# Performance work log

Measured on AMD Instinct MI355X. Metric: run time of the kernel, lower is better.

The kernel has to match this reference:

```python
import jax, jax.numpy as jnp
import numpy as np
import math

IN_CH, KEY_SIZE, VALUE_SIZE = 512, 64, 64
N, T = 4, 4096

def setup_inputs() -> dict:
    key = jax.random.key(0)
    ks = jax.random.split(key, 7)
    s_in = 1.0 / math.sqrt(IN_CH)
    return {
        "x": jax.random.normal(ks[0], (N, T, IN_CH), dtype=jnp.float32),
        "Wq": jax.random.uniform(ks[1], (IN_CH, KEY_SIZE), jnp.float32, -s_in, s_in),
        "bq": jax.random.uniform(ks[2], (KEY_SIZE,), jnp.float32, -s_in, s_in),
        "Wk": jax.random.uniform(ks[3], (IN_CH, KEY_SIZE), jnp.float32, -s_in, s_in),
        "bk": jax.random.uniform(ks[4], (KEY_SIZE,), jnp.float32, -s_in, s_in),
        "Wv": jax.random.uniform(ks[5], (IN_CH, VALUE_SIZE), jnp.float32, -s_in, s_in),
        "bv": jax.random.uniform(ks[6], (VALUE_SIZE,), jnp.float32, -s_in, s_in),
    }

def reference(x, Wq, bq, Wk, bk, Wv, bv):
    # x: [N, T, C]
    Tlen = x.shape[1]
    q = x @ Wq + bq              # [N, T, K]
    k = x @ Wk + bk              # [N, T, K]
    v = x @ Wv + bv              # [N, T, V]
    logits = jnp.einsum('ntk,nsk->nts', q, k)  # [N, T, T]
    # causal mask: strict upper triangle -> -inf (applied BEFORE scaling, as in the original)
    causal = jnp.tril(jnp.ones((Tlen, Tlen), dtype=bool))
    logits = jnp.where(causal, logits, -jnp.inf)
    scale = 1.0 / math.sqrt(Wq.shape[1])
    attn = jax.nn.softmax(logits * scale, axis=-1)
    read = jnp.einsum('nts,nsv->ntv', attn, v)  # [N, T, V]
    return jnp.concatenate((x, read), axis=2)   # [N, T, C+V]
```

## Files before the change

kernel.cpp:

```cpp
#include <hip/hip_runtime.h>
#include <stdint.h>

typedef __attribute__((ext_vector_type(8))) short bf16x8;
typedef __attribute__((ext_vector_type(4))) float f32x4;
typedef __attribute__((ext_vector_type(4))) unsigned short u16x4;
typedef unsigned short u16;

#define NBATCH 4
#define SEQ    4096
#define CIN    512
#define HD     64
#define OC     576
#define NROW   (NBATCH * SEQ)
#define KVB    262144

__device__ __forceinline__ float b2f(u16 u) {
    union { uint32_t i; float f; } w; w.i = ((uint32_t)u) << 16; return w.f;
}
__device__ __forceinline__ u16 f2b(float f) {
    union { float f; uint32_t i; } w; w.f = f;
    uint32_t r = w.i + 0x7fffu + ((w.i >> 16) & 1u);
    return (u16)(r >> 16);
}
__device__ __forceinline__ uint32_t cvtpk_bf16(float a, float b) {
    uint32_t r;
    asm("v_cvt_pk_bf16_f32 %0, %1, %2" : "=v"(r) : "v"(a), "v"(b));
    return r;
}

__global__ void prep_wt(const float* __restrict__ Wq, const float* __restrict__ Wk,
                        const float* __restrict__ Wv, u16* __restrict__ wt) {
    int row = blockIdx.x;
    int g = row >> 6, j = row & 63;
    const float* W = (g == 0) ? Wq : (g == 1) ? Wk : Wv;
    for (int k = threadIdx.x; k < CIN; k += blockDim.x)
        wt[row * CIN + k] = f2b(W[k * HD + j]);
}

__global__ __launch_bounds__(256) void proj(
    const float* __restrict__ x, const u16* __restrict__ wt,
    const float* __restrict__ bq, const float* __restrict__ bk, const float* __restrict__ bv,
    u16* __restrict__ qb, u16* __restrict__ kbuf, u16* __restrict__ vtb,
    float* __restrict__ out)
{
    __shared__ __align__(16) float xs[16 * 512];

    int tid = threadIdx.x;
    int lane = tid & 63, w = tid >> 6;
    int m = lane & 15, quad = lane >> 4;
    int r0 = blockIdx.x * 16;

    {
        int rw = w >> 1;
        int pp = (w & 1) * 64 + lane;
#pragma unroll
        for (int k = 0; k < 8; k++) {
            int r = k * 2 + rw;
            int g = pp ^ (r & 15);
            const float* src = x + (size_t)(r0 + r) * CIN + g * 4;
            float* dst = xs + (size_t)(k * 256 + w * 64 + lane) * 4;
            __builtin_amdgcn_global_load_lds(
                (const __attribute__((address_space(1))) void*)src,
                (__attribute__((address_space(3))) void*)dst, 16, 0, 0);
        }
    }
    __syncthreads();

    int ntb = w * 3;

    f32x4 acc[3];
#pragma unroll
    for (int i = 0; i < 3; i++) acc[i] = (f32x4){0.f, 0.f, 0.f, 0.f};

    const float* xrow = xs + (size_t)m * 512;

#pragma unroll
    for (int c = 0; c < 16; c++) {
        int L0 = c * 8 + quad * 2;
        f32x4 va = *(const f32x4*)(xrow + (size_t)((L0 ^ m) * 4));
        f32x4 vb = *(const f32x4*)(xrow + (size_t)(((L0 + 1) ^ m) * 4));
        bf16x8 a;
#pragma unroll
        for (int j = 0; j < 4; j++) { a[j] = (short)f2b(va[j]); a[4 + j] = (short)f2b(vb[j]); }
#pragma unroll
        for (int t = 0; t < 3; t++) {
            int nt = ntb + t;
            bf16x8 b = *(const bf16x8*)(wt + (size_t)(nt * 16 + m) * CIN + c * 32 + quad * 8);
            acc[t] = __builtin_amdgcn_mfma_f32_16x16x32_bf16(a, b, acc[t], 0, 0, 0);
        }
    }

#pragma unroll
    for (int k = 0; k < 8; k++) {
        int G = k * 256 + tid;
        int r = G >> 7, p = G & 127;
        f32x4 v = *(const f32x4*)(xs + (size_t)G * 4);
        int col = (p ^ (r & 15)) * 4;
        *(f32x4*)(out + (size_t)(r0 + r) * OC + col) = v;
    }

    int n  = r0 >> 12;
    int tl = r0 & (SEQ - 1);

    const float SCQ = 0.125f * 1.44269504088896f;

#pragma unroll
    for (int t = 0; t < 3; t++) {
        int nt = ntb + t;
        int bi = (nt & 3) * 16 + m;
        if (nt < 4) {
            float biasq = bq[bi];
#pragma unroll
            for (int reg = 0; reg < 4; reg++) {
                size_t r = (size_t)(r0 + quad * 4 + reg);
                qb[r * HD + bi] = f2b((acc[t][reg] + biasq) * SCQ);
            }
        } else if (nt < 8) {
            float biask = bk[bi];
            u16* kbase = kbuf + (size_t)n * KVB
                       + (((size_t)(tl >> 4) * 8 + (bi >> 3)) * 16) * 8 + (bi & 7);
#pragma unroll
            for (int reg = 0; reg < 4; reg++) {
                int mkey = quad * 4 + reg;
                kbase[(size_t)mkey * 8] = f2b(acc[t][reg] + biask);
            }
        } else {
            float biasv = bv[bi];
            u16x4 pk;
#pragma unroll
            for (int reg = 0; reg < 4; reg++) pk[reg] = f2b(acc[t][reg] + biasv);
            int key0 = tl + quad * 4;
            size_t off = ((((size_t)(bi >> 4) * 128 + (key0 >> 5)) * 4
                           + ((key0 >> 3) & 3)) * 16 + (bi & 15)) * 8 + (key0 & 7);
            *(u16x4*)(vtb + (size_t)n * KVB + off) = pk;
        }
    }
}

__global__ __launch_bounds__(512, 2) void attn(
    const u16* __restrict__ qb, const u16* __restrict__ kbuf,
    const u16* __restrict__ vtb, float* __restrict__ out)
{
    __shared__ __align__(16) union {
        short p[8][16 * 72];
        float o[8][16][68];
    } lu;
    __shared__ float ldsm[8][16];
    __shared__ float ldsl[8][16];

    int tid = threadIdx.x;
    int lane = tid & 63, w = tid >> 6;
    int m = lane & 15, quad = lane >> 4;

    int idx = blockIdx.x;
    int xcd = idx & 7;
    int batch = xcd >> 1;
    int sub = (idx >> 3) * 2 + (xcd & 1);
    int jj = 127 - sub;
    int t0 = jj * 32;
    int nkb = (jj >> 1) + 1;
    int lastkb = nkb - 1;

    const u16* kpb = kbuf + (size_t)batch * KVB;
    const u16* vpb = vtb + (size_t)batch * KVB;

    bf16x8 ones;
#pragma unroll
    for (int i = 0; i < 8; i++) ones[i] = (short)0x3F80;

    const u16* qpb = qb + (size_t)(batch * SEQ + t0 + m) * HD + quad * 8;
    bf16x8 q0[2], q1[2];
#pragma unroll
    for (int q = 0; q < 2; q++) {
        q0[q] = *(const bf16x8*)(qpb + (size_t)(q * 16) * HD);
        q1[q] = *(const bf16x8*)(qpb + (size_t)(q * 16) * HD + 32);
    }

    float mst[2];
    f32x4 o[2][4], ol[2];
#pragma unroll
    for (int q = 0; q < 2; q++) {
        mst[q] = -1e30f;
        ol[q] = (f32x4){0.f, 0.f, 0.f, 0.f};
#pragma unroll
        for (int nt = 0; nt < 4; nt++) o[q][nt] = (f32x4){0.f, 0.f, 0.f, 0.f};
    }

    int cnt = (nkb > w) ? ((nkb - w + 7) >> 3) : 0;
    int kb = w;
    short* pw = &lu.p[w][0];

    bf16x8 k0[4], k1[4];
#pragma unroll
    for (int st = 0; st < 4; st++) {
        k0[st] = *(const bf16x8*)(kpb + (size_t)((kb * 4 + st) * 8 + quad) * 128 + m * 8);
        k1[st] = *(const bf16x8*)(kpb + (size_t)((kb * 4 + st) * 8 + quad + 4) * 128 + m * 8);
    }

    for (int it = 0; it < cnt; it++, kb += 8) {
        int s0 = kb * 64;
        bool diag = (kb == lastkb);

        bf16x8 vf0[4], vf1[4];
#pragma unroll
        for (int nt = 0; nt < 4; nt++) {
            vf0[nt] = *(const bf16x8*)(vpb + (size_t)((nt * 128 + (s0 >> 5)) * 4 + quad) * 128 + m * 8);
            vf1[nt] = *(const bf16x8*)(vpb + (size_t)((nt * 128 + (s0 >> 5) + 1) * 4 + quad) * 128 + m * 8);
        }

        f32x4 s[2][4];
#pragma unroll
        for (int q = 0; q < 2; q++)
#pragma unroll
            for (int st = 0; st < 4; st++) {
                f32x4 a = (f32x4){0.f, 0.f, 0.f, 0.f};
                a = __builtin_amdgcn_mfma_f32_16x16x32_bf16(k0[st], q0[q], a, 0, 0, 0);
                a = __builtin_amdgcn_mfma_f32_16x16x32_bf16(k1[st], q1[q], a, 0, 0, 0);
                s[q][st] = a;
            }

        if (it + 1 < cnt) {
            int kn = kb + 8;
#pragma unroll
            for (int st = 0; st < 4; st++) {
                k0[st] = *(const bf16x8*)(kpb + (size_t)((kn * 4 + st) * 8 + quad) * 128 + m * 8);
                k1[st] = *(const bf16x8*)(kpb + (size_t)((kn * 4 + st) * 8 + quad + 4) * 128 + m * 8);
            }
        }

        if (diag) {
#pragma unroll
            for (int q = 0; q < 2; q++)
#pragma unroll
                for (int st = 0; st < 4; st++)
#pragma unroll
                    for (int r = 0; r < 4; r++) {
                        int key = s0 + st * 16 + quad * 4 + r;
                        if (key > t0 + q * 16 + m) s[q][st][r] = -1e30f;
                    }
        }

        bf16x8 pf0[2], pf1[2];
#pragma unroll
        for (int q = 0; q < 2; q++) {
            float mx = -1e30f;
#pragma unroll
            for (int st = 0; st < 4; st++) {
                float a01 = fmaxf(s[q][st][0], s[q][st][1]);
                float a23 = fmaxf(s[q][st][2], s[q][st][3]);
                mx = fmaxf(mx, fmaxf(a01, a23));
            }
            mx = fmaxf(mx, __shfl_xor(mx, 16, 64));
            mx = fmaxf(mx, __shfl_xor(mx, 32, 64));

            if (__any(mx > mst[q] + 8.0f)) {
                float mn = fmaxf(mst[q], mx);
                float al = exp2f(mst[q] - mn);
#pragma unroll
                for (int nt = 0; nt < 4; nt++)
#pragma unroll
                    for (int r = 0; r < 4; r++) o[q][nt][r] *= al;
                ol[q][0] *= al;
                mst[q] = mn;
            }

#pragma unroll
            for (int st = 0; st < 4; st++) {
                float e0 = exp2f(s[q][st][0] - mst[q]);
                float e1 = exp2f(s[q][st][1] - mst[q]);
                float e2 = exp2f(s[q][st][2] - mst[q]);
                float e3 = exp2f(s[q][st][3] - mst[q]);
                uint2 pk2;
                pk2.x = cvtpk_bf16(e0, e1);
                pk2.y = cvtpk_bf16(e2, e3);
                *(uint2*)(pw + m * 72 + st * 16 + quad * 4) = pk2;
            }
            __asm__ volatile("" ::: "memory");
            pf0[q] = *(const bf16x8*)(pw + m * 72 + quad * 8);
            pf1[q] = *(const bf16x8*)(pw + m * 72 + 32 + quad * 8);
            __asm__ volatile("" ::: "memory");
        }

#pragma unroll
        for (int q = 0; q < 2; q++) {
#pragma unroll
            for (int nt = 0; nt < 4; nt++) {
                o[q][nt] = __builtin_amdgcn_mfma_f32_16x16x32_bf16(vf0[nt], pf0[q], o[q][nt], 0, 0, 0);
                o[q][nt] = __builtin_amdgcn_mfma_f32_16x16x32_bf16(vf1[nt], pf1[q], o[q][nt], 0, 0, 0);
            }
            ol[q] = __builtin_amdgcn_mfma_f32_16x16x32_bf16(ones, pf0[q], ol[q], 0, 0, 0);
            ol[q] = __builtin_amdgcn_mfma_f32_16x16x32_bf16(ones, pf1[q], ol[q], 0, 0, 0);
        }
    }

    __syncthreads();

#pragma unroll
    for (int q = 0; q < 2; q++) {
        if (quad == 0) { ldsm[w][m] = mst[q]; ldsl[w][m] = ol[q][0]; }
#pragma unroll
        for (int nt = 0; nt < 4; nt++)
            *(f32x4*)&lu.o[w][m][nt * 16 + quad * 4] = o[q][nt];
        __syncthreads();

        if (tid < 256) {
            int t = tid >> 4, vg = tid & 15;
            float mmax = -1e30f;
#pragma unroll
            for (int u = 0; u < 8; u++) mmax = fmaxf(mmax, ldsm[u][t]);
            float L = 0.f;
            f32x4 acc = (f32x4){0.f, 0.f, 0.f, 0.f};
#pragma unroll
            for (int u = 0; u < 8; u++) {
                float c = exp2f(ldsm[u][t] - mmax);
                L += ldsl[u][t] * c;
                f32x4 ov = *(const f32x4*)&lu.o[u][t][vg * 4];
#pragma unroll
                for (int i2 = 0; i2 < 4; i2++) acc[i2] += ov[i2] * c;
            }
            float inv = 1.0f / L;
            f32x4 res;
#pragma unroll
            for (int i2 = 0; i2 < 4; i2++) res[i2] = acc[i2] * inv;
            *(f32x4*)(out + (size_t)(batch * SEQ + t0 + q * 16 + t) * OC + CIN + vg * 4) = res;
        }
        __syncthreads();
    }
}

extern "C" void kernel_launch(void* const* d_in, const int* in_sizes, int n_in,
                              void* d_out, int out_size, void* d_ws, size_t ws_size,
                              hipStream_t stream) {
    const float* x  = (const float*)d_in[0];
    const float* Wq = (const float*)d_in[1];
    const float* bq = (const float*)d_in[2];
    const float* Wk = (const float*)d_in[3];
    const float* bk = (const float*)d_in[4];
    const float* Wv = (const float*)d_in[5];
    const float* bv = (const float*)d_in[6];
    float* out = (float*)d_out;

    u16* ws  = (u16*)d_ws;
    u16* wt  = ws;
    u16* qb  = ws + 131072;
    u16* kb  = qb + 16384 * 64;
    u16* vtb = kb + 16384 * 64;

    prep_wt<<<dim3(192), dim3(256), 0, stream>>>(Wq, Wk, Wv, wt);
    proj<<<dim3(1024), dim3(256), 0, stream>>>(x, wt, bq, bk, bv, qb, kb, vtb, out);
    attn<<<dim3(512), dim3(512), 0, stream>>>(qb, kb, vtb, out);
}
```

Baseline: 140.6 us.

## Process 32 rows per projection block and retile weights for coalesced MFMA loads

The projection kernel now handles 32 rows per block instead of 16, so each loaded weight fragment feeds two MFMAs and weight traffic is halved. The bf16 weight matrix is rearranged in prep_wt so each MFMA B-operand load is contiguous across lanes. The fp32-to-bf16 conversion uses packed v_cvt_pk_bf16_f32 instructions. In exchange, LDS use doubles to 64KB per block and the grid halves, which lowers occupancy and parallelism.

New measurement: 129.1 us. 8.2% less time.

```diff
diff --git a/kernel.cpp b/kernel.cpp
--- a/kernel.cpp
+++ b/kernel.cpp
@@ -33,8 +33,12 @@
     int row = blockIdx.x;
     int g = row >> 6, j = row & 63;
     const float* W = (g == 0) ? Wq : (g == 1) ? Wk : Wv;
-    for (int k = threadIdx.x; k < CIN; k += blockDim.x)
-        wt[row * CIN + k] = f2b(W[k * HD + j]);
+    int nt = row >> 4, m = row & 15;
+    for (int k = threadIdx.x; k < CIN; k += blockDim.x) {
+        int c = k >> 5, qd = (k >> 3) & 3, jj = k & 7;
+        size_t off = ((size_t)(nt * 16 + c) * 64 + qd * 16 + m) * 8 + jj;
+        wt[off] = f2b(W[k * HD + j]);
+    }
 }
 
 __global__ __launch_bounds__(256) void proj(
@@ -43,21 +47,21 @@
     u16* __restrict__ qb, u16* __restrict__ kbuf, u16* __restrict__ vtb,
     float* __restrict__ out)
 {
-    __shared__ __align__(16) float xs[16 * 512];
+    __shared__ __align__(16) float xs[32 * 512];
 
     int tid = threadIdx.x;
     int lane = tid & 63, w = tid >> 6;
     int m = lane & 15, quad = lane >> 4;
-    int r0 = blockIdx.x * 16;
+    int r0b = blockIdx.x * 32;
 
     {
         int rw = w >> 1;
         int pp = (w & 1) * 64 + lane;
 #pragma unroll
-        for (int k = 0; k < 8; k++) {
+        for (int k = 0; k < 16; k++) {
             int r = k * 2 + rw;
             int g = pp ^ (r & 15);
-            const float* src = x + (size_t)(r0 + r) * CIN + g * 4;
+            const float* src = x + (size_t)(r0b + r) * CIN + g * 4;
             float* dst = xs + (size_t)(k * 256 + w * 64 + lane) * 4;
             __builtin_amdgcn_global_load_lds(
                 (const __attribute__((address_space(1))) void*)src,
@@ -68,71 +72,92 @@
 
     int ntb = w * 3;
 
-    f32x4 acc[3];
-#pragma unroll
-    for (int i = 0; i < 3; i++) acc[i] = (f32x4){0.f, 0.f, 0.f, 0.f};
-
-    const float* xrow = xs + (size_t)m * 512;
+    f32x4 acc0[3], acc1[3];
+#pragma unroll
+    for (int i = 0; i < 3; i++) {
+        acc0[i] = (f32x4){0.f, 0.f, 0.f, 0.f};
+        acc1[i] = (f32x4){0.f, 0.f, 0.f, 0.f};
+    }
+
+    const float* xrow0 = xs + (size_t)m * 512;
+    const float* xrow1 = xs + (size_t)(16 + m) * 512;
 
 #pragma unroll
     for (int c = 0; c < 16; c++) {
         int L0 = c * 8 + quad * 2;
-        f32x4 va = *(const f32x4*)(xrow + (size_t)((L0 ^ m) * 4));
-        f32x4 vb = *(const f32x4*)(xrow + (size_t)(((L0 + 1) ^ m) * 4));
-        bf16x8 a;
-#pragma unroll
-        for (int j = 0; j < 4; j++) { a[j] = (short)f2b(va[j]); a[4 + j] = (short)f2b(vb[j]); }
+        f32x4 va0 = *(const f32x4*)(xrow0 + (size_t)((L0 ^ m) * 4));
+        f32x4 vb0 = *(const f32x4*)(xrow0 + (size_t)(((L0 + 1) ^ m) * 4));
+        f32x4 va1 = *(const f32x4*)(xrow1 + (size_t)((L0 ^ m) * 4));
+        f32x4 vb1 = *(const f32x4*)(xrow1 + (size_t)(((L0 + 1) ^ m) * 4));
+        bf16x8 a0, a1;
+        {
+            uint32_t* p0 = (uint32_t*)&a0;
+            p0[0] = cvtpk_bf16(va0[0], va0[1]);
+            p0[1] = cvtpk_bf16(va0[2], va0[3]);
+            p0[2] = cvtpk_bf16(vb0[0], vb0[1]);
+            p0[3] = cvtpk_bf16(vb0[2], vb0[3]);
+            uint32_t* p1 = (uint32_t*)&a1;
+            p1[0] = cvtpk_bf16(va1[0], va1[1]);
+            p1[1] = cvtpk_bf16(va1[2], va1[3]);
+            p1[2] = cvtpk_bf16(vb1[0], vb1[1]);
+            p1[3] = cvtpk_bf16(vb1[2], vb1[3]);
+        }
 #pragma unroll
         for (int t = 0; t < 3; t++) {
             int nt = ntb + t;
-            bf16x8 b = *(const bf16x8*)(wt + (size_t)(nt * 16 + m) * CIN + c * 32 + quad * 8);
-            acc[t] = __builtin_amdgcn_mfma_f32_16x16x32_bf16(a, b, acc[t], 0, 0, 0);
-        }
-    }
-
-#pragma unroll
-    for (int k = 0; k < 8; k++) {
+            bf16x8 b = *(const bf16x8*)(wt + ((size_t)(nt * 16 + c) * 64 + quad * 16 + m) * 8);
+            acc0[t] = __builtin_amdgcn_mfma_f32_16x16x32_bf16(a0, b, acc0[t], 0, 0, 0);
+            acc1[t] = __builtin_amdgcn_mfma_f32_16x16x32_bf16(a1, b, acc1[t], 0, 0, 0);
+        }
+    }
+
+#pragma unroll
+    for (int k = 0; k < 16; k++) {
         int G = k * 256 + tid;
         int r = G >> 7, p = G & 127;
         f32x4 v = *(const f32x4*)(xs + (size_t)G * 4);
         int col = (p ^ (r & 15)) * 4;
-        *(f32x4*)(out + (size_t)(r0 + r) * OC + col) = v;
-    }
-
-    int n  = r0 >> 12;
-    int tl = r0 & (SEQ - 1);
+        *(f32x4*)(out + (size_t)(r0b + r) * OC + col) = v;
+    }
 
     const float SCQ = 0.125f * 1.44269504088896f;
 
 #pragma unroll
-    for (int t = 0; t < 3; t++) {
-        int nt = ntb + t;
-        int bi = (nt & 3) * 16 + m;
-        if (nt < 4) {
-            float biasq = bq[bi];
-#pragma unroll
-            for (int reg = 0; reg < 4; reg++) {
-                size_t r = (size_t)(r0 + quad * 4 + reg);
-                qb[r * HD + bi] = f2b((acc[t][reg] + biasq) * SCQ);
-            }
-        } else if (nt < 8) {
-            float biask = bk[bi];
-            u16* kbase = kbuf + (size_t)n * KVB
-                       + (((size_t)(tl >> 4) * 8 + (bi >> 3)) * 16) * 8 + (bi & 7);
-#pragma unroll
-            for (int reg = 0; reg < 4; reg++) {
-                int mkey = quad * 4 + reg;
-                kbase[(size_t)mkey * 8] = f2b(acc[t][reg] + biask);
-            }
-        } else {
-            float biasv = bv[bi];
-            u16x4 pk;
-#pragma unroll
-            for (int reg = 0; reg < 4; reg++) pk[reg] = f2b(acc[t][reg] + biasv);
-            int key0 = tl + quad * 4;
-            size_t off = ((((size_t)(bi >> 4) * 128 + (key0 >> 5)) * 4
-                           + ((key0 >> 3) & 3)) * 16 + (bi & 15)) * 8 + (key0 & 7);
-            *(u16x4*)(vtb + (size_t)n * KVB + off) = pk;
+    for (int tt = 0; tt < 2; tt++) {
+        int r0 = r0b + tt * 16;
+        int n  = r0 >> 12;
+        int tl = r0 & (SEQ - 1);
+#pragma unroll
+        for (int t = 0; t < 3; t++) {
+            f32x4 acc = tt ? acc1[t] : acc0[t];
+            int nt = ntb + t;
+            int bi = (nt & 3) * 16 + m;
+            if (nt < 4) {
+                float biasq = bq[bi];
+#pragma unroll
+                for (int reg = 0; reg < 4; reg++) {
+                    size_t r = (size_t)(r0 + quad * 4 + reg);
+                    qb[r * HD + bi] = f2b((acc[reg] + biasq) * SCQ);
+                }
+            } else if (nt < 8) {
+                float biask = bk[bi];
+                u16* kbase = kbuf + (size_t)n * KVB
+                           + (((size_t)(tl >> 4) * 8 + (bi >> 3)) * 16) * 8 + (bi & 7);
+#pragma unroll
+                for (int reg = 0; reg < 4; reg++) {
+                    int mkey = quad * 4 + reg;
+                    kbase[(size_t)mkey * 8] = f2b(acc[reg] + biask);
+                }
+            } else {
+                float biasv = bv[bi];
+                u16x4 pk;
+#pragma unroll
+                for (int reg = 0; reg < 4; reg++) pk[reg] = f2b(acc[reg] + biasv);
+                int key0 = tl + quad * 4;
+                size_t off = ((((size_t)(bi >> 4) * 128 + (key0 >> 5)) * 4
+                               + ((key0 >> 3) & 3)) * 16 + (bi & 15)) * 8 + (key0 & 7);
+                *(u16x4*)(vtb + (size_t)n * KVB + off) = pk;
+            }
         }
     }
 }
@@ -347,6 +372,6 @@
     u16* vtb = kb + 16384 * 64;
 
     prep_wt<<<dim3(192), dim3(256), 0, stream>>>(Wq, Wk, Wv, wt);
-    proj<<<dim3(1024), dim3(256), 0, stream>>>(x, wt, bq, bk, bv, qb, kb, vtb, out);
+    proj<<<dim3(512), dim3(256), 0, stream>>>(x, wt, bq, bk, bv, qb, kb, vtb, out);
     attn<<<dim3(512), dim3(512), 0, stream>>>(qb, kb, vtb, out);
 }
```
